# Performance work log

Measured on AMD Instinct MI355X. Metric: run time of the kernel, lower is better.

Reference implementation:

```python
import jax, jax.numpy as jnp
import numpy as np

VOCAB = 32000
EMB = 256
UNITS = 1024


def setup_inputs() -> dict:
    key = jax.random.key(0)
    ks = jax.random.split(key, 6)
    B, S = 128, 256
    x = jax.random.randint(ks[0], (B, S), 0, VOCAB, dtype=jnp.int32)
    hidden = jnp.zeros((B, UNITS), jnp.float32)
    # Parameters (Keras GRU v2, reset_after=True): kernel W [EMB, 3*UNITS],
    # recurrent kernel U [UNITS, 3*UNITS], bias b [2, 3*UNITS] (input bias, recurrent bias)
    emb = jax.random.normal(ks[1], (VOCAB, EMB), jnp.float32) * 0.05
    W = jax.random.normal(ks[2], (EMB, 3 * UNITS), jnp.float32) * (1.0 / np.sqrt(EMB))
    U = jax.random.normal(ks[3], (UNITS, 3 * UNITS), jnp.float32) * (1.0 / np.sqrt(UNITS))
    b = jnp.zeros((2, 3 * UNITS), jnp.float32)
    return {"x": x, "hidden": hidden, "emb": emb, "W": W, "U": U, "b": b}


def _gru_seq(xp, hidden, U, b_rec):
    # xp: [S, B, 3H] precomputed input projections (incl. input bias)
    H = hidden.shape[-1]

    def step(h, xt):
        rec = h @ U + b_rec                       # [B, 3H]
        xz, xr, xh = xt[:, :H], xt[:, H:2 * H], xt[:, 2 * H:]
        rz, rr, rh = rec[:, :H], rec[:, H:2 * H], rec[:, 2 * H:]
        z = jax.nn.sigmoid(xz + rz)
        r = jax.nn.sigmoid(xr + rr)
        hh = jnp.tanh(xh + r * rh)                # reset_after=True
        h_new = z * h + (1.0 - z) * hh
        return h_new, h_new

    state, outs = jax.lax.scan(step, hidden, xp)
    return outs, state


def reference(x, hidden, emb, W, U, b):
    xe = emb[x]                                   # [B, S, EMB]
    # Precompute all input-side projections in one big GEMM
    xp = jnp.einsum('bse,eh->bsh', xe, W) + b[0]  # [B, S, 3H]
    xp = jnp.swapaxes(xp, 0, 1)                   # [S, B, 3H]
    outs, state = _gru_seq(xp, hidden, U, b[1])
    output = jnp.swapaxes(outs, 0, 1)             # [B, S, H]
    return output, state
```

## Files before the change

kernel.cpp:

```cpp
#include <hip/hip_runtime.h>

#define B_   128
#define S_   256
#define EMB_ 256
#define H_   1024
#define NH3  3072

#define G_      8
#define NW      32
#define MG      16
#define HS      32
#define THREADS 768

typedef _Float16 f16;
typedef _Float16 h8 __attribute__((ext_vector_type(8)));
typedef float    f4 __attribute__((ext_vector_type(4)));
typedef unsigned long long u64;

__global__ void gather_kernel(const int* __restrict__ x, const float* __restrict__ emb,
                              f16* __restrict__ xe16) {
  int m = blockIdx.x, k = threadIdx.x;
  int b = m & 127, s = m >> 7;
  int row = x[b * S_ + s];
  xe16[m * EMB_ + k] = (f16)emb[row * EMB_ + k];
}

__global__ void transpose_cvt(const float* __restrict__ in, f16* __restrict__ out,
                              int K, int N) {
  __shared__ float tile[32][33];
  int n0 = blockIdx.x * 32, k0 = blockIdx.y * 32;
  int tx = threadIdx.x & 31, ty = threadIdx.x >> 5;
#pragma unroll
  for (int i = 0; i < 4; ++i)
    tile[ty + 8 * i][tx] = in[(k0 + ty + 8 * i) * N + n0 + tx];
  __syncthreads();
#pragma unroll
  for (int i = 0; i < 4; ++i)
    out[(n0 + ty + 8 * i) * K + k0 + tx] = (f16)tile[tx][ty + 8 * i];
}

__launch_bounds__(THREADS, 3)
__global__ void gru_kernel(const f16* __restrict__ xe16, const f16* __restrict__ Ut,
                           const f16* __restrict__ Wt, const float* __restrict__ hidden,
                           const float* __restrict__ bvec, float* __restrict__ out,
                           f16* __restrict__ h16, int* __restrict__ flags) {
  __shared__ f16   h_lds[MG * H_];
  __shared__ f16   xe_lds[2][MG * EMB_];
  __shared__ float recS[4][MG][100];
  __shared__ float recU[4][MG][36];

  const int tid = threadIdx.x;
  const int bid = blockIdx.x;
  const int g   = bid & 7;
  const int w   = bid >> 3;
  const int gb0 = g * MG;
  const int hc0 = w * HS;

  const int lane = tid & 63;
  const int wv   = tid >> 6;
  const int ksp  = wv & 3;
  const int cp   = wv >> 2;
  const int ln   = lane & 15;
  const int klo  = lane >> 4;
  const int bl   = tid >> 5;
  const int jl   = tid & 31;

  int* gflags = flags + g * NW;

  h8 uf0[8], uf1[8], wf0[2], wf1[2];
  {
    const f16* u0 = Ut + (size_t)(cp * H_ + hc0 + ln) * H_ + ksp * 256 + klo * 8;
    const f16* u1 = u0 + (size_t)16 * H_;
#pragma unroll
    for (int kt = 0; kt < 8; ++kt) { uf0[kt] = *(const h8*)(u0 + kt * 32);
                                     uf1[kt] = *(const h8*)(u1 + kt * 32); }
    const f16* w0 = Wt + (size_t)(cp * H_ + hc0 + ln) * EMB_ + ksp * 64 + klo * 8;
    const f16* w1 = w0 + 16 * EMB_;
#pragma unroll
    for (int kt = 0; kt < 2; ++kt) { wf0[kt] = *(const h8*)(w0 + kt * 32);
                                     wf1[kt] = *(const h8*)(w1 + kt * 32); }
  }
#pragma unroll
  for (int kt = 0; kt < 8; ++kt) { asm volatile("" : "+v"(uf0[kt])); asm volatile("" : "+v"(uf1[kt])); }
  asm volatile("" : "+v"(wf0[0]), "+v"(wf0[1]), "+v"(wf1[0]), "+v"(wf1[1]));

  float hprev = 0.f, bz = 0.f, brr = 0.f, bxh = 0.f, brh = 0.f;
  size_t obase = 0, soff = 0;
  if (tid < 512) {
    int col = hc0 + jl;
    bz  = bvec[col] + bvec[NH3 + col];
    brr = bvec[H_ + col] + bvec[NH3 + H_ + col];
    bxh = bvec[2 * H_ + col];
    brh = bvec[NH3 + 2 * H_ + col];
    hprev = hidden[(size_t)(gb0 + bl) * H_ + col];
    obase = ((size_t)(gb0 + bl) * S_) * H_ + col;
    soff  = (size_t)(gb0 + bl) * H_ + col;
  }

  for (int idx = tid; idx < MG * H_ / 4; idx += THREADS) {
    int r = idx >> 8, c4 = idx & 255;
    float4 hv = ((const float4*)(hidden + (size_t)(gb0 + r) * H_))[c4];
    unsigned lo = ((unsigned)__builtin_bit_cast(unsigned short, (f16)hv.y) << 16)
                |  (unsigned)__builtin_bit_cast(unsigned short, (f16)hv.x);
    unsigned hi = ((unsigned)__builtin_bit_cast(unsigned short, (f16)hv.w) << 16)
                |  (unsigned)__builtin_bit_cast(unsigned short, (f16)hv.z);
    uint2 pk = {lo, hi};
    *(uint2*)((char*)h_lds + r * 2048 + ((c4 * 8) ^ ((r & 7) << 4))) = pk;
  }
  for (int idx = tid; idx < MG * EMB_ / 8; idx += THREADS) {
    uint4 v = ((const uint4*)(xe16 + (size_t)gb0 * EMB_))[idx];
    int r = idx >> 5, c = idx & 31;
    *(uint4*)((char*)xe_lds[0] + r * 512 + ((c * 16) ^ ((r & 7) << 4))) = v;
  }
  __syncthreads();

  for (int t = 0; t < S_; ++t) {
    if (t > 0) {
      const u64* src = (const u64*)(h16 + (size_t)(t & 1) * (B_ * H_) + (size_t)gb0 * H_);
      u64 v0 = __hip_atomic_load(src + tid,               __ATOMIC_RELAXED, __HIP_MEMORY_SCOPE_AGENT);
      u64 v1 = __hip_atomic_load(src + tid + THREADS,     __ATOMIC_RELAXED, __HIP_MEMORY_SCOPE_AGENT);
      u64 v2 = __hip_atomic_load(src + tid + 2 * THREADS, __ATOMIC_RELAXED, __HIP_MEMORY_SCOPE_AGENT);
      u64 v3 = __hip_atomic_load(src + tid + 3 * THREADS, __ATOMIC_RELAXED, __HIP_MEMORY_SCOPE_AGENT);
      u64 v4 = __hip_atomic_load(src + tid + 4 * THREADS, __ATOMIC_RELAXED, __HIP_MEMORY_SCOPE_AGENT);
      u64 v5 = 0;
      if (tid < 256)
        v5 = __hip_atomic_load(src + 3840 + tid, __ATOMIC_RELAXED, __HIP_MEMORY_SCOPE_AGENT);
      { int idx = tid;               int r = idx >> 8, c = idx & 255;
        *(u64*)((char*)h_lds + r * 2048 + ((c * 8) ^ ((r & 7) << 4))) = v0; }
      { int idx = tid + THREADS;     int r = idx >> 8, c = idx & 255;
        *(u64*)((char*)h_lds + r * 2048 + ((c * 8) ^ ((r & 7) << 4))) = v1; }
      { int idx = tid + 2 * THREADS; int r = idx >> 8, c = idx & 255;
        *(u64*)((char*)h_lds + r * 2048 + ((c * 8) ^ ((r & 7) << 4))) = v2; }
      { int idx = tid + 3 * THREADS; int r = idx >> 8, c = idx & 255;
        *(u64*)((char*)h_lds + r * 2048 + ((c * 8) ^ ((r & 7) << 4))) = v3; }
      { int idx = tid + 4 * THREADS; int r = idx >> 8, c = idx & 255;
        *(u64*)((char*)h_lds + r * 2048 + ((c * 8) ^ ((r & 7) << 4))) = v4; }
      if (tid < 256) {
        int idx = 3840 + tid;        int r = idx >> 8, c = idx & 255;
        *(u64*)((char*)h_lds + r * 2048 + ((c * 8) ^ ((r & 7) << 4))) = v5;
      }
      __syncthreads();
    }

    f4 a0 = {0.f,0.f,0.f,0.f}, a1 = {0.f,0.f,0.f,0.f};
    f4 a2 = {0.f,0.f,0.f,0.f}, a3 = {0.f,0.f,0.f,0.f};
    const char* hb = (const char*)h_lds + ln * 2048;
    const char* xb = (const char*)xe_lds[t & 1] + ln * 512;
    const int rm = (ln & 7) << 4;
#pragma unroll
    for (int kt = 0; kt < 8; ++kt) {
      h8 a = *(const h8*)(hb + ((ksp * 512 + kt * 64 + klo * 16) ^ rm));
      a0 = __builtin_amdgcn_mfma_f32_16x16x32_f16(a, uf0[kt], a0, 0, 0, 0);
      a1 = __builtin_amdgcn_mfma_f32_16x16x32_f16(a, uf1[kt], a1, 0, 0, 0);
    }
#pragma unroll
    for (int kt = 0; kt < 2; ++kt) {
      h8 aw = *(const h8*)(xb + ((ksp * 128 + kt * 64 + klo * 16) ^ rm));
      a2 = __builtin_amdgcn_mfma_f32_16x16x32_f16(aw, wf0[kt], a2, 0, 0, 0);
      a3 = __builtin_amdgcn_mfma_f32_16x16x32_f16(aw, wf1[kt], a3, 0, 0, 0);
    }
#pragma unroll
    for (int j = 0; j < 4; ++j) {
      int r = klo * 4 + j;
      if (cp < 2) {
        recS[ksp][r][cp * 32 + ln]      = a0[j] + a2[j];
        recS[ksp][r][cp * 32 + 16 + ln] = a1[j] + a3[j];
      } else {
        recS[ksp][r][64 + ln] = a2[j];
        recS[ksp][r][80 + ln] = a3[j];
        recU[ksp][r][ln]      = a0[j];
        recU[ksp][r][16 + ln] = a1[j];
      }
    }
    __syncthreads();

    float outv = 0.f;
    if (tid < 512) {
      float az = recS[0][bl][jl] + recS[1][bl][jl] + recS[2][bl][jl] + recS[3][bl][jl] + bz;
      float ar = recS[0][bl][32+jl] + recS[1][bl][32+jl] + recS[2][bl][32+jl] + recS[3][bl][32+jl] + brr;
      float xh = recS[0][bl][64+jl] + recS[1][bl][64+jl] + recS[2][bl][64+jl] + recS[3][bl][64+jl] + bxh;
      float rhu = recU[0][bl][jl] + recU[1][bl][jl] + recU[2][bl][jl] + recU[3][bl][jl] + brh;
      float z  = 1.f / (1.f + __expf(-az));
      float r  = 1.f / (1.f + __expf(-ar));
      float hh = 1.f - 2.f / (1.f + __expf(2.f * (xh + r * rhu)));
      float hn = z * hprev + (1.f - z) * hh;
      hprev = hn; outv = hn;
      if (t < S_ - 1) {
        unsigned short hb16 = __builtin_bit_cast(unsigned short, (f16)hn);
        __hip_atomic_store((unsigned short*)(h16 + (size_t)((t + 1) & 1) * (B_ * H_)) + soff,
                           hb16, __ATOMIC_RELAXED, __HIP_MEMORY_SCOPE_AGENT);
      }
    }
    if (t == S_ - 1) {
      if (tid < 512) {
        out[obase + (size_t)t * H_] = outv;
        out[(size_t)B_ * S_ * H_ + soff] = outv;
      }
      break;
    }

    asm volatile("s_waitcnt vmcnt(0)" ::: "memory");
    __syncthreads();
    if (tid == 0)
      __hip_atomic_store(&gflags[w], t + 1, __ATOMIC_RELAXED, __HIP_MEMORY_SCOPE_AGENT);

    if (tid < 512) {
      out[obase + (size_t)t * H_] = outv;
    } else {
      const uint4* src = (const uint4*)(xe16 + ((size_t)(t + 1) * B_ + gb0) * EMB_);
      char* dst = (char*)xe_lds[(t + 1) & 1];
#pragma unroll
      for (int i = 0; i < 2; ++i) {
        int idx = (tid - 512) * 2 + i;
        uint4 v = src[idx];
        int r = idx >> 5, c = idx & 31;
        *(uint4*)(dst + r * 512 + ((c * 16) ^ ((r & 7) << 4))) = v;
      }
    }
    if (wv == 0) {
      const int need = t + 1;
      for (;;) {
        int f = __hip_atomic_load(&gflags[lane & 31], __ATOMIC_RELAXED, __HIP_MEMORY_SCOPE_AGENT);
        if (__all(f >= need)) break;
      }
    }
    __syncthreads();
  }
}

extern "C" void kernel_launch(void* const* d_in, const int* in_sizes, int n_in,
                              void* d_out, int out_size, void* d_ws, size_t ws_size,
                              hipStream_t stream) {
  const int*   x      = (const int*)  d_in[0];
  const float* hidden = (const float*)d_in[1];
  const float* emb    = (const float*)d_in[2];
  const float* W      = (const float*)d_in[3];
  const float* U      = (const float*)d_in[4];
  const float* bvec   = (const float*)d_in[5];
  float* out = (float*)d_out;

  char* ws = (char*)d_ws;
  f16* Ut    = (f16*)(ws);
  f16* Wt    = (f16*)(ws + 6291456);
  f16* xe16  = (f16*)(ws + 7864320);
  f16* h16   = (f16*)(ws + 24641536);
  int* flags = (int*)(ws + 25165824);

  hipMemsetAsync(flags, 0, 1024, stream);
  hipLaunchKernelGGL(transpose_cvt, dim3(NH3 / 32, H_ / 32), dim3(256), 0, stream,
                     U, Ut, H_, NH3);
  hipLaunchKernelGGL(transpose_cvt, dim3(NH3 / 32, EMB_ / 32), dim3(256), 0, stream,
                     W, Wt, EMB_, NH3);
  hipLaunchKernelGGL(gather_kernel, dim3(B_ * S_), dim3(EMB_), 0, stream, x, emb, xe16);

  void* args[] = { (void*)&xe16, (void*)&Ut, (void*)&Wt, (void*)&hidden,
                   (void*)&bvec, (void*)&out, (void*)&h16, (void*)&flags };
  hipLaunchCooperativeKernel(reinterpret_cast<void*>(gru_kernel),
                             dim3(G_ * NW), dim3(THREADS), args, 0, stream);
}
```

Measured before the change: 861.0 us.

## Replace global barrier with per-slice flag waits and overlapped hidden-state loads

Instead of wave 0 spinning until all 32 workgroup flags reach the step count, each wave waits only on the flags of the producer slices whose hidden-state columns it needs, then loads those columns directly into LDS. This removes the separate all-to-all barrier followed by a bulk reload, letting waves begin fetching data as soon as their specific producers finish. It adds s_sleep-based polling per wave, which increases the number of flag loads.

```diff
diff --git a/kernel.cpp b/kernel.cpp
--- a/kernel.cpp
+++ b/kernel.cpp
@@ -16,6 +16,9 @@
 typedef _Float16 h8 __attribute__((ext_vector_type(8)));
 typedef float    f4 __attribute__((ext_vector_type(4)));
 typedef unsigned long long u64;
+
+#define AL64(pp) __hip_atomic_load((pp), __ATOMIC_RELAXED, __HIP_MEMORY_SCOPE_AGENT)
+#define ALI(pp)  __hip_atomic_load((pp), __ATOMIC_RELAXED, __HIP_MEMORY_SCOPE_AGENT)
 
 __global__ void gather_kernel(const int* __restrict__ x, const float* __restrict__ emb,
                               f16* __restrict__ xe16) {
@@ -114,34 +117,11 @@
   }
   __syncthreads();
 
+  const int s0p = wv, s1p = wv + 12, s2p = wv + 24;
+  const int pr  = lane >> 2;
+  const int pc  = (lane & 3) * 2;
+
   for (int t = 0; t < S_; ++t) {
-    if (t > 0) {
-      const u64* src = (const u64*)(h16 + (size_t)(t & 1) * (B_ * H_) + (size_t)gb0 * H_);
-      u64 v0 = __hip_atomic_load(src + tid,               __ATOMIC_RELAXED, __HIP_MEMORY_SCOPE_AGENT);
-      u64 v1 = __hip_atomic_load(src + tid + THREADS,     __ATOMIC_RELAXED, __HIP_MEMORY_SCOPE_AGENT);
-      u64 v2 = __hip_atomic_load(src + tid + 2 * THREADS, __ATOMIC_RELAXED, __HIP_MEMORY_SCOPE_AGENT);
-      u64 v3 = __hip_atomic_load(src + tid + 3 * THREADS, __ATOMIC_RELAXED, __HIP_MEMORY_SCOPE_AGENT);
-      u64 v4 = __hip_atomic_load(src + tid + 4 * THREADS, __ATOMIC_RELAXED, __HIP_MEMORY_SCOPE_AGENT);
-      u64 v5 = 0;
-      if (tid < 256)
-        v5 = __hip_atomic_load(src + 3840 + tid, __ATOMIC_RELAXED, __HIP_MEMORY_SCOPE_AGENT);
-      { int idx = tid;               int r = idx >> 8, c = idx & 255;
-        *(u64*)((char*)h_lds + r * 2048 + ((c * 8) ^ ((r & 7) << 4))) = v0; }
-      { int idx = tid + THREADS;     int r = idx >> 8, c = idx & 255;
-        *(u64*)((char*)h_lds + r * 2048 + ((c * 8) ^ ((r & 7) << 4))) = v1; }
-      { int idx = tid + 2 * THREADS; int r = idx >> 8, c = idx & 255;
-        *(u64*)((char*)h_lds + r * 2048 + ((c * 8) ^ ((r & 7) << 4))) = v2; }
-      { int idx = tid + 3 * THREADS; int r = idx >> 8, c = idx & 255;
-        *(u64*)((char*)h_lds + r * 2048 + ((c * 8) ^ ((r & 7) << 4))) = v3; }
-      { int idx = tid + 4 * THREADS; int r = idx >> 8, c = idx & 255;
-        *(u64*)((char*)h_lds + r * 2048 + ((c * 8) ^ ((r & 7) << 4))) = v4; }
-      if (tid < 256) {
-        int idx = 3840 + tid;        int r = idx >> 8, c = idx & 255;
-        *(u64*)((char*)h_lds + r * 2048 + ((c * 8) ^ ((r & 7) << 4))) = v5;
-      }
-      __syncthreads();
-    }
-
     f4 a0 = {0.f,0.f,0.f,0.f}, a1 = {0.f,0.f,0.f,0.f};
     f4 a2 = {0.f,0.f,0.f,0.f}, a3 = {0.f,0.f,0.f,0.f};
     const char* hb = (const char*)h_lds + ln * 2048;
@@ -155,9 +135,9 @@
     }
 #pragma unroll
     for (int kt = 0; kt < 2; ++kt) {
-      h8 aw = *(const h8*)(xb + ((ksp * 128 + kt * 64 + klo * 16) ^ rm));
-      a2 = __builtin_amdgcn_mfma_f32_16x16x32_f16(aw, wf0[kt], a2, 0, 0, 0);
-      a3 = __builtin_amdgcn_mfma_f32_16x16x32_f16(aw, wf1[kt], a3, 0, 0, 0);
+      h8 a = *(const h8*)(xb + ((ksp * 128 + kt * 64 + klo * 16) ^ rm));
+      a2 = __builtin_amdgcn_mfma_f32_16x16x32_f16(a, wf0[kt], a2, 0, 0, 0);
+      a3 = __builtin_amdgcn_mfma_f32_16x16x32_f16(a, wf1[kt], a3, 0, 0, 0);
     }
 #pragma unroll
     for (int j = 0; j < 4; ++j) {
@@ -217,11 +197,33 @@
         *(uint4*)(dst + r * 512 + ((c * 16) ^ ((r & 7) << 4))) = v;
       }
     }
-    if (wv == 0) {
+
+    {
       const int need = t + 1;
-      for (;;) {
-        int f = __hip_atomic_load(&gflags[lane & 31], __ATOMIC_RELAXED, __HIP_MEMORY_SCOPE_AGENT);
-        if (__all(f >= need)) break;
+      const u64* hbuf = (const u64*)(h16 + (size_t)((t + 1) & 1) * (B_ * H_));
+      const int rowu = (gb0 + pr) * 256;
+      for (;;) { int f = ALI(&gflags[s0p]); if (f >= need) break; __builtin_amdgcn_s_sleep(1); }
+      for (;;) { int f = ALI(&gflags[s1p]); if (f >= need) break; __builtin_amdgcn_s_sleep(1); }
+      if (wv < 8)
+        for (;;) { int f = ALI(&gflags[s2p]); if (f >= need) break; __builtin_amdgcn_s_sleep(1); }
+      u64 va0 = AL64(hbuf + rowu + s0p * 8 + pc);
+      u64 va1 = AL64(hbuf + rowu + s0p * 8 + pc + 1);
+      u64 vb0 = AL64(hbuf + rowu + s1p * 8 + pc);
+      u64 vb1 = AL64(hbuf + rowu + s1p * 8 + pc + 1);
+      u64 vc0 = 0, vc1 = 0;
+      if (wv < 8) {
+        vc0 = AL64(hbuf + rowu + s2p * 8 + pc);
+        vc1 = AL64(hbuf + rowu + s2p * 8 + pc + 1);
+      }
+      char* hd = (char*)h_lds + pr * 2048;
+      const int prm = (pr & 7) << 4;
+      *(u64*)(hd + ((s0p * 64 + pc * 8    ) ^ prm)) = va0;
+      *(u64*)(hd + ((s0p * 64 + pc * 8 + 8) ^ prm)) = va1;
+      *(u64*)(hd + ((s1p * 64 + pc * 8    ) ^ prm)) = vb0;
+      *(u64*)(hd + ((s1p * 64 + pc * 8 + 8) ^ prm)) = vb1;
+      if (wv < 8) {
+        *(u64*)(hd + ((s2p * 64 + pc * 8    ) ^ prm)) = vc0;
+        *(u64*)(hd + ((s2p * 64 + pc * 8 + 8) ^ prm)) = vc1;
       }
     }
     __syncthreads();
```

Result: slower. 1.064 ms (+23.6%).
